# Performance work log

Hardware: AMD Instinct MI355X
Metric: run time of the kernel (lower is better)

## Reference

```python
import jax, jax.numpy as jnp
import numpy as np

NUM_USERS = 100000
NUM_ITEMS = 200000
D = 128          # embedding_dim
K = 4            # num interest heads
B = 4096
H = 256          # history length
H1, H2 = 512, 256  # hidden_units


def setup_inputs() -> dict:
    key = jax.random.key(0)
    ks = jax.random.split(key, 10)
    inp = {
        "user_ids": jax.random.randint(ks[0], (B,), 0, NUM_USERS),
        "candidate_items": jax.random.randint(ks[1], (B,), 0, NUM_ITEMS),
        "history_items": jax.random.randint(ks[2], (B, H), 0, NUM_ITEMS),
        "item_table": jax.random.normal(ks[3], (NUM_ITEMS, D), dtype=jnp.float32) * 0.05,
        "Wp": jax.random.normal(ks[4], (D, K), dtype=jnp.float32) * (1.0 / np.sqrt(D)),
        "W1": jax.random.normal(ks[5], (2 * D, H1), dtype=jnp.float32) * (1.0 / np.sqrt(2 * D)),
        "b1": jnp.zeros((H1,), dtype=jnp.float32),
        "W2": jax.random.normal(ks[6], (H1, H2), dtype=jnp.float32) * (1.0 / np.sqrt(H1)),
        "b2": jnp.zeros((H2,), dtype=jnp.float32),
        "W3": jax.random.normal(ks[7], (H2, 1), dtype=jnp.float32) * (1.0 / np.sqrt(H2)),
        "b3": jnp.zeros((1,), dtype=jnp.float32),
    }
    return inp


def reference(user_ids, candidate_items, history_items, item_table, Wp,
              W1, b1, W2, b2, W3, b3):
    # user_ids is unused by the original forward (user_emb never applied)
    item_vecs = item_table[history_items]          # (B, H, D)
    cand_vec = item_table[candidate_items]         # (B, D)

    # per-interest attention scores, softmax over history axis
    scores = jnp.einsum('bhd,dk->bhk', item_vecs, Wp)   # (B, H, K)
    scores = jax.nn.softmax(scores, axis=1)

    # softmax-weighted pooling -> K interest vectors per user
    interest_vectors = jnp.einsum('bhk,bhd->bkd', scores, item_vecs)  # (B, K, D)

    # similarity to candidate, pick best interest (data-dependent gather)
    sim_scores = jnp.einsum('bkd,bd->bk', interest_vectors, cand_vec)  # (B, K)
    best_idx = jnp.argmax(sim_scores, axis=-1)                          # (B,)
    selected = jnp.take_along_axis(
        interest_vectors, best_idx[:, None, None], axis=1)[:, 0, :]    # (B, D)

    # MLP tail: [2D -> 512] ReLU [512 -> 256] ReLU [256 -> 1], sigmoid
    x = jnp.concatenate([selected, cand_vec], axis=-1)  # (B, 2D)
    x = jax.nn.relu(x @ W1 + b1)
    x = jax.nn.relu(x @ W2 + b2)
    out = (x @ W3 + b3)[:, 0]                            # (B,)
    return jax.nn.sigmoid(out)
```

## Files before the change

### kernel.cpp

```cpp
#include <hip/hip_runtime.h>
#include <hip/hip_bf16.h>
#include <math.h>

#define B_SZ   4096
#define H_LEN  256
#define D_DIM  128
#define K_HEADS 4
#define H1_DIM 512
#define H2_DIM 256

#define CH     64
#define NCH    4
#define TPAD   132

typedef __attribute__((ext_vector_type(8))) short bf16x8;
typedef __attribute__((ext_vector_type(4))) float f32x4;

__global__ __launch_bounds__(256, 4) void interest_kernel(
    const int*   __restrict__ cand_ids,
    const int*   __restrict__ hist,
    const float* __restrict__ table,
    const float* __restrict__ Wp,
    __hip_bfloat16* __restrict__ Xbf)
{
    __shared__ float tile[CH * TPAD];
    __shared__ float wpt[K_HEADS * D_DIM];
    __shared__ float exps4[CH * 4];
    __shared__ float candv[D_DIM];
    __shared__ int   rowids[H_LEN];
    __shared__ float lsumW[16];
    __shared__ float simred[4][K_HEADS];
    __shared__ int   bestk;

    const int b    = blockIdx.x;
    const int t    = threadIdx.x;
    const int lane = t & 63, w = t >> 6;
    const int r    = t >> 2, q = t & 3;
    const int d    = t & 127, half = t >> 7;

    if (t < D_DIM) {
        float4 w4 = ((const float4*)Wp)[t];
        wpt[0 * D_DIM + t] = w4.x;
        wpt[1 * D_DIM + t] = w4.y;
        wpt[2 * D_DIM + t] = w4.z;
        wpt[3 * D_DIM + t] = w4.w;
    }
    const int cand = cand_ids[b];
    if (t >= 128 && t < 160) {
        int c = t - 128;
        ((float4*)candv)[c] = ((const float4*)(table + (long long)cand * D_DIM))[c];
    }
    rowids[t] = hist[(long long)b * H_LEN + t];

    float a0 = 0.f, a1 = 0.f, a2 = 0.f, a3 = 0.f;
    float l0 = 0.f, l1 = 0.f, l2 = 0.f, l3 = 0.f;

    for (int c = 0; c < NCH; ++c) {
        __syncthreads();

        const int   row = rowids[(c << 6) + r];
        const float* rp = table + (long long)row * D_DIM + (q << 2);
        float4 v0 = *(const float4*)(rp + 0 * 16);
        float4 v1 = *(const float4*)(rp + 1 * 16);
        float4 v2 = *(const float4*)(rp + 2 * 16);
        float4 v3 = *(const float4*)(rp + 3 * 16);
        float4 v4 = *(const float4*)(rp + 4 * 16);
        float4 v5 = *(const float4*)(rp + 5 * 16);
        float4 v6 = *(const float4*)(rp + 6 * 16);
        float4 v7 = *(const float4*)(rp + 7 * 16);

        float s0 = 0.f, s1 = 0.f, s2 = 0.f, s3 = 0.f;
        float4 va;
        #define DO_J(J, VV)                                                     \
        {   va = VV;                                                            \
            const int cb = (q << 2) + (J << 4);                                 \
            float4 w0 = *(const float4*)(wpt + 0 * D_DIM + cb);                 \
            float4 w1 = *(const float4*)(wpt + 1 * D_DIM + cb);                 \
            float4 w2 = *(const float4*)(wpt + 2 * D_DIM + cb);                 \
            float4 w3 = *(const float4*)(wpt + 3 * D_DIM + cb);                 \
            s0 += va.x * w0.x + va.y * w0.y + va.z * w0.z + va.w * w0.w;        \
            s1 += va.x * w1.x + va.y * w1.y + va.z * w1.z + va.w * w1.w;        \
            s2 += va.x * w2.x + va.y * w2.y + va.z * w2.z + va.w * w2.w;        \
            s3 += va.x * w3.x + va.y * w3.y + va.z * w3.z + va.w * w3.w;        \
            *(float4*)(tile + r * TPAD + cb) = va;                              \
        }
        DO_J(0, v0) DO_J(1, v1) DO_J(2, v2) DO_J(3, v3)
        DO_J(4, v4) DO_J(5, v5) DO_J(6, v6) DO_J(7, v7)
        #undef DO_J

        s0 += __shfl_xor(s0, 1); s0 += __shfl_xor(s0, 2);
        s1 += __shfl_xor(s1, 1); s1 += __shfl_xor(s1, 2);
        s2 += __shfl_xor(s2, 1); s2 += __shfl_xor(s2, 2);
        s3 += __shfl_xor(s3, 1); s3 += __shfl_xor(s3, 2);

        float e0 = expf(s0), e1 = expf(s1), e2 = expf(s2), e3 = expf(s3);
        if (q == 0) ((float4*)exps4)[r] = make_float4(e0, e1, e2, e3);

        float t0 = e0, t1 = e1, t2 = e2, t3 = e3;
        #pragma unroll
        for (int off = 4; off <= 32; off <<= 1) {
            t0 += __shfl_xor(t0, off);
            t1 += __shfl_xor(t1, off);
            t2 += __shfl_xor(t2, off);
            t3 += __shfl_xor(t3, off);
        }
        l0 += t0; l1 += t1; l2 += t2; l3 += t3;

        __syncthreads();

        #pragma unroll 8
        for (int i = 0; i < 32; ++i) {
            int hl = (half << 5) + i;
            float4 e4 = ((const float4*)exps4)[hl];
            float  vv = tile[hl * TPAD + d];
            a0 += e4.x * vv; a1 += e4.y * vv; a2 += e4.z * vv; a3 += e4.w * vv;
        }
    }

    __syncthreads();
    float* partBp = tile;
    float* ivbufp = tile + 512;

    if (half == 1) ((float4*)partBp)[d] = make_float4(a0, a1, a2, a3);
    if (lane == 0) ((float4*)lsumW)[w]  = make_float4(l0, l1, l2, l3);
    __syncthreads();

    float s0 = 0.f, s1 = 0.f, s2 = 0.f, s3 = 0.f;
    if (half == 0) {
        float4 pb = ((const float4*)partBp)[d];
        float4 L0 = ((const float4*)lsumW)[0];
        float4 L1 = ((const float4*)lsumW)[1];
        float4 L2 = ((const float4*)lsumW)[2];
        float4 L3 = ((const float4*)lsumW)[3];
        float i0 = 1.f / (L0.x + L1.x + L2.x + L3.x);
        float i1 = 1.f / (L0.y + L1.y + L2.y + L3.y);
        float i2 = 1.f / (L0.z + L1.z + L2.z + L3.z);
        float i3 = 1.f / (L0.w + L1.w + L2.w + L3.w);
        a0 = (a0 + pb.x) * i0;
        a1 = (a1 + pb.y) * i1;
        a2 = (a2 + pb.z) * i2;
        a3 = (a3 + pb.w) * i3;
        ((float4*)ivbufp)[d] = make_float4(a0, a1, a2, a3);
        float cd = candv[d];
        s0 = a0 * cd; s1 = a1 * cd; s2 = a2 * cd; s3 = a3 * cd;
    }
    #pragma unroll
    for (int off = 32; off >= 1; off >>= 1) {
        s0 += __shfl_xor(s0, off);
        s1 += __shfl_xor(s1, off);
        s2 += __shfl_xor(s2, off);
        s3 += __shfl_xor(s3, off);
    }
    if (lane == 0) {
        simred[w][0] = s0; simred[w][1] = s1;
        simred[w][2] = s2; simred[w][3] = s3;
    }
    __syncthreads();

    if (t == 0) {
        float sim[4];
        #pragma unroll
        for (int k = 0; k < 4; ++k)
            sim[k] = simred[0][k] + simred[1][k] + simred[2][k] + simred[3][k];
        int best = 0;
        #pragma unroll
        for (int k = 1; k < 4; ++k) if (sim[k] > sim[best]) best = k;
        bestk = best;
    }
    __syncthreads();

    __hip_bfloat16* xrow = Xbf + (long long)b * (2 * D_DIM);
    if (t < 128) xrow[t] = __float2bfloat16(ivbufp[t * 4 + bestk]);
    else         xrow[t] = __float2bfloat16(candv[t - 128]);
}

__global__ __launch_bounds__(256) void convert_weights(
    const float* __restrict__ W1, const float* __restrict__ W2,
    __hip_bfloat16* __restrict__ W1t, __hip_bfloat16* __restrict__ W2t)
{
    int idx = blockIdx.x * 256 + threadIdx.x;
    if (idx < 2 * D_DIM * H1_DIM) {
        int n = idx >> 8, k = idx & 255;
        W1t[idx] = __float2bfloat16(W1[k * H1_DIM + n]);
    } else {
        int j = idx - 2 * D_DIM * H1_DIM;
        int n = j >> 9, k = j & 511;
        W2t[j] = __float2bfloat16(W2[k * H2_DIM + n]);
    }
}

template<int N, int K, bool OUT_BF16>
__global__ __launch_bounds__(256) void mfma_mlp(
    const __hip_bfloat16* __restrict__ A,
    const __hip_bfloat16* __restrict__ Bt,
    const float* __restrict__ bias,
    void* __restrict__ Cout)
{
    const int t    = threadIdx.x;
    const int wave = t >> 6, lane = t & 63;
    const int lm   = lane & 15, quad = lane >> 4;
    const int n0   = blockIdx.x * 16;
    const int m0   = blockIdx.y * 64 + wave * 16;

    const __hip_bfloat16* Ap = A  + (long long)(m0 + lm) * K + quad * 8;
    const __hip_bfloat16* Bp = Bt + (long long)(n0 + lm) * K + quad * 8;

    f32x4 acc = {0.f, 0.f, 0.f, 0.f};
    for (int kc = 0; kc < K; kc += 256) {
        bf16x8 af[8], bfr[8];
        #pragma unroll
        for (int it = 0; it < 8; ++it) {
            af[it]  = *(const bf16x8*)(Ap + kc + it * 32);
            bfr[it] = *(const bf16x8*)(Bp + kc + it * 32);
        }
        #pragma unroll
        for (int it = 0; it < 8; ++it)
            acc = __builtin_amdgcn_mfma_f32_16x16x32_bf16(af[it], bfr[it], acc, 0, 0, 0);
    }

    const int n  = n0 + lm;
    const float bv = bias[n];
    #pragma unroll
    for (int i = 0; i < 4; ++i) {
        int m = m0 + quad * 4 + i;
        float v = fmaxf(acc[i] + bv, 0.f);
        if (OUT_BF16)
            ((__hip_bfloat16*)Cout)[(long long)m * N + n] = __float2bfloat16(v);
        else
            ((float*)Cout)[(long long)m * N + n] = v;
    }
}

__global__ __launch_bounds__(256) void head_kernel(
    const float* __restrict__ H2buf,
    const float* __restrict__ W3,
    const float* __restrict__ b3,
    float*       __restrict__ out)
{
    const int b = blockIdx.x * 256 + threadIdx.x;
    const float4* hp = (const float4*)(H2buf + (long long)b * H2_DIM);
    const float4* wp = (const float4*)W3;
    float acc = 0.f;
    #pragma unroll 8
    for (int i = 0; i < H2_DIM / 4; ++i) {
        float4 h = hp[i], wv = wp[i];
        acc += h.x * wv.x + h.y * wv.y + h.z * wv.z + h.w * wv.w;
    }
    float z = acc + b3[0];
    out[b] = 1.f / (1.f + expf(-z));
}

extern "C" void kernel_launch(void* const* d_in, const int* in_sizes, int n_in,
                              void* d_out, int out_size, void* d_ws, size_t ws_size,
                              hipStream_t stream) {
    const int*   cand  = (const int*)  d_in[1];
    const int*   hist  = (const int*)  d_in[2];
    const float* table = (const float*)d_in[3];
    const float* Wp    = (const float*)d_in[4];
    const float* W1    = (const float*)d_in[5];
    const float* b1    = (const float*)d_in[6];
    const float* W2    = (const float*)d_in[7];
    const float* b2    = (const float*)d_in[8];
    const float* W3    = (const float*)d_in[9];
    const float* b3    = (const float*)d_in[10];
    float* out = (float*)d_out;

    char* p = (char*)d_ws;
    __hip_bfloat16* Xbf  = (__hip_bfloat16*)p;                  p += (size_t)B_SZ * 2 * D_DIM * 2;
    __hip_bfloat16* Hc1  = (__hip_bfloat16*)p;                  p += (size_t)B_SZ * H1_DIM * 2;
    float*          Hc2  = (float*)p;                           p += (size_t)B_SZ * H2_DIM * 4;
    __hip_bfloat16* W1t  = (__hip_bfloat16*)p;                  p += (size_t)H1_DIM * 2 * D_DIM * 2;
    __hip_bfloat16* W2t  = (__hip_bfloat16*)p;

    convert_weights<<<(2 * D_DIM * H1_DIM + H1_DIM * H2_DIM) / 256, 256, 0, stream>>>(
        W1, W2, W1t, W2t);
    interest_kernel<<<B_SZ, 256, 0, stream>>>(cand, hist, table, Wp, Xbf);
    mfma_mlp<H1_DIM, 2 * D_DIM, true><<<dim3(H1_DIM / 16, B_SZ / 64), 256, 0, stream>>>(
        Xbf, W1t, b1, Hc1);
    mfma_mlp<H2_DIM, H1_DIM, false><<<dim3(H2_DIM / 16, B_SZ / 64), 256, 0, stream>>>(
        Hc1, W2t, b2, Hc2);
    head_kernel<<<B_SZ / 256, 256, 0, stream>>>(Hc2, W3, b3, out);
}
```

Before: 274.8 us.

## Make interest pooling wave-local with register prefetch and fuse weight conversion

The interest kernel is restructured so that each wave owns its own 16-row tile slice and does its own weighted pooling. This removes the block-wide barriers inside the history loop, and cross-wave partials are reduced once at the end. The next chunk of gathered table rows is prefetched into registers while the current chunk is being processed, to hide gather latency. The separate weight-conversion kernel is folded into extra blocks of the interest kernel, saving one launch. The cost is higher register pressure from the double-buffered float4 arrays, which may reduce occupancy.

```diff
diff --git a/kernel.cpp b/kernel.cpp
--- a/kernel.cpp
+++ b/kernel.cpp
@@ -8,9 +8,6 @@
 #define K_HEADS 4
 #define H1_DIM 512
 #define H2_DIM 256
-
-#define CH     64
-#define NCH    4
 #define TPAD   132
 
 typedef __attribute__((ext_vector_type(8))) short bf16x8;
@@ -21,13 +18,30 @@
     const int*   __restrict__ hist,
     const float* __restrict__ table,
     const float* __restrict__ Wp,
+    const float* __restrict__ W1,
+    const float* __restrict__ W2,
+    __hip_bfloat16* __restrict__ W1t,
+    __hip_bfloat16* __restrict__ W2t,
     __hip_bfloat16* __restrict__ Xbf)
 {
-    __shared__ float tile[CH * TPAD];
+    if (blockIdx.x >= B_SZ) {
+        int idx = (blockIdx.x - B_SZ) * 256 + threadIdx.x;
+        if (idx < 2 * D_DIM * H1_DIM) {
+            int n = idx >> 8, k = idx & 255;
+            W1t[idx] = __float2bfloat16(W1[k * H1_DIM + n]);
+        } else {
+            int j = idx - 2 * D_DIM * H1_DIM;
+            int n = j >> 9, k = j & 511;
+            W2t[j] = __float2bfloat16(W2[k * H2_DIM + n]);
+        }
+        return;
+    }
+
+    __shared__ float tile[4 * 16 * TPAD];
     __shared__ float wpt[K_HEADS * D_DIM];
-    __shared__ float exps4[CH * 4];
+    __shared__ float exps4[4 * 16 * 4];
     __shared__ float candv[D_DIM];
-    __shared__ int   rowids[H_LEN];
+    __shared__ float ivbuf[D_DIM * 4];
     __shared__ float lsumW[16];
     __shared__ float simred[4][K_HEADS];
     __shared__ int   bestk;
@@ -35,8 +49,10 @@
     const int b    = blockIdx.x;
     const int t    = threadIdx.x;
     const int lane = t & 63, w = t >> 6;
-    const int r    = t >> 2, q = t & 3;
-    const int d    = t & 127, half = t >> 7;
+    const int r    = lane >> 2;
+    const int q    = lane & 3;
+    const int d0   = lane, d1 = lane + 64;
+    const int wtile = w * (16 * TPAD);
 
     if (t < D_DIM) {
         float4 w4 = ((const float4*)Wp)[t];
@@ -50,84 +66,97 @@
         int c = t - 128;
         ((float4*)candv)[c] = ((const float4*)(table + (long long)cand * D_DIM))[c];
     }
-    rowids[t] = hist[(long long)b * H_LEN + t];
-
-    float a0 = 0.f, a1 = 0.f, a2 = 0.f, a3 = 0.f;
-    float l0 = 0.f, l1 = 0.f, l2 = 0.f, l3 = 0.f;
-
-    for (int c = 0; c < NCH; ++c) {
-        __syncthreads();
-
-        const int   row = rowids[(c << 6) + r];
-        const float* rp = table + (long long)row * D_DIM + (q << 2);
-        float4 v0 = *(const float4*)(rp + 0 * 16);
-        float4 v1 = *(const float4*)(rp + 1 * 16);
-        float4 v2 = *(const float4*)(rp + 2 * 16);
-        float4 v3 = *(const float4*)(rp + 3 * 16);
-        float4 v4 = *(const float4*)(rp + 4 * 16);
-        float4 v5 = *(const float4*)(rp + 5 * 16);
-        float4 v6 = *(const float4*)(rp + 6 * 16);
-        float4 v7 = *(const float4*)(rp + 7 * 16);
-
+    __syncthreads();
+
+    int ids[4];
+    {
+        const long long hb = (long long)b * H_LEN + w * 64 + r;
+        #pragma unroll
+        for (int c = 0; c < 4; ++c) ids[c] = hist[hb + c * 16];
+    }
+
+    float accA[4] = {0.f, 0.f, 0.f, 0.f};
+    float accB[4] = {0.f, 0.f, 0.f, 0.f};
+    float lsum[4] = {0.f, 0.f, 0.f, 0.f};
+
+    float4 v[8];
+    {
+        const float* rp = table + (long long)ids[0] * D_DIM + (q << 2);
+        #pragma unroll
+        for (int j = 0; j < 8; ++j) v[j] = *(const float4*)(rp + j * 16);
+    }
+
+    #pragma unroll
+    for (int c = 0; c < 4; ++c) {
         float s0 = 0.f, s1 = 0.f, s2 = 0.f, s3 = 0.f;
-        float4 va;
-        #define DO_J(J, VV)                                                     \
-        {   va = VV;                                                            \
-            const int cb = (q << 2) + (J << 4);                                 \
-            float4 w0 = *(const float4*)(wpt + 0 * D_DIM + cb);                 \
-            float4 w1 = *(const float4*)(wpt + 1 * D_DIM + cb);                 \
-            float4 w2 = *(const float4*)(wpt + 2 * D_DIM + cb);                 \
-            float4 w3 = *(const float4*)(wpt + 3 * D_DIM + cb);                 \
-            s0 += va.x * w0.x + va.y * w0.y + va.z * w0.z + va.w * w0.w;        \
-            s1 += va.x * w1.x + va.y * w1.y + va.z * w1.z + va.w * w1.w;        \
-            s2 += va.x * w2.x + va.y * w2.y + va.z * w2.z + va.w * w2.w;        \
-            s3 += va.x * w3.x + va.y * w3.y + va.z * w3.z + va.w * w3.w;        \
-            *(float4*)(tile + r * TPAD + cb) = va;                              \
-        }
-        DO_J(0, v0) DO_J(1, v1) DO_J(2, v2) DO_J(3, v3)
-        DO_J(4, v4) DO_J(5, v5) DO_J(6, v6) DO_J(7, v7)
-        #undef DO_J
+        #pragma unroll
+        for (int j = 0; j < 8; ++j) {
+            const int cb = (q << 2) + (j << 4);
+            float4 va = v[j];
+            float4 w0 = *(const float4*)(wpt + 0 * D_DIM + cb);
+            float4 w1 = *(const float4*)(wpt + 1 * D_DIM + cb);
+            float4 w2 = *(const float4*)(wpt + 2 * D_DIM + cb);
+            float4 w3 = *(const float4*)(wpt + 3 * D_DIM + cb);
+            s0 += va.x * w0.x + va.y * w0.y + va.z * w0.z + va.w * w0.w;
+            s1 += va.x * w1.x + va.y * w1.y + va.z * w1.z + va.w * w1.w;
+            s2 += va.x * w2.x + va.y * w2.y + va.z * w2.z + va.w * w2.w;
+            s3 += va.x * w3.x + va.y * w3.y + va.z * w3.z + va.w * w3.w;
+            *(float4*)(tile + wtile + r * TPAD + cb) = va;
+        }
+
+        float4 vn[8];
+        if (c < 3) {
+            const float* rp = table + (long long)ids[c + 1] * D_DIM + (q << 2);
+            #pragma unroll
+            for (int j = 0; j < 8; ++j) vn[j] = *(const float4*)(rp + j * 16);
+        }
 
         s0 += __shfl_xor(s0, 1); s0 += __shfl_xor(s0, 2);
         s1 += __shfl_xor(s1, 1); s1 += __shfl_xor(s1, 2);
         s2 += __shfl_xor(s2, 1); s2 += __shfl_xor(s2, 2);
         s3 += __shfl_xor(s3, 1); s3 += __shfl_xor(s3, 2);
-
         float e0 = expf(s0), e1 = expf(s1), e2 = expf(s2), e3 = expf(s3);
-        if (q == 0) ((float4*)exps4)[r] = make_float4(e0, e1, e2, e3);
-
-        float t0 = e0, t1 = e1, t2 = e2, t3 = e3;
-        #pragma unroll
-        for (int off = 4; off <= 32; off <<= 1) {
-            t0 += __shfl_xor(t0, off);
-            t1 += __shfl_xor(t1, off);
-            t2 += __shfl_xor(t2, off);
-            t3 += __shfl_xor(t3, off);
-        }
-        l0 += t0; l1 += t1; l2 += t2; l3 += t3;
-
-        __syncthreads();
-
-        #pragma unroll 8
-        for (int i = 0; i < 32; ++i) {
-            int hl = (half << 5) + i;
-            float4 e4 = ((const float4*)exps4)[hl];
-            float  vv = tile[hl * TPAD + d];
-            a0 += e4.x * vv; a1 += e4.y * vv; a2 += e4.z * vv; a3 += e4.w * vv;
-        }
-    }
-
-    __syncthreads();
-    float* partBp = tile;
-    float* ivbufp = tile + 512;
-
-    if (half == 1) ((float4*)partBp)[d] = make_float4(a0, a1, a2, a3);
-    if (lane == 0) ((float4*)lsumW)[w]  = make_float4(l0, l1, l2, l3);
+        if (q == 0) ((float4*)exps4)[w * 16 + r] = make_float4(e0, e1, e2, e3);
+        lsum[0] += e0; lsum[1] += e1; lsum[2] += e2; lsum[3] += e3;
+
+        #pragma unroll
+        for (int h = 0; h < 16; ++h) {
+            float4 e4 = ((const float4*)exps4)[w * 16 + h];
+            float  p0 = tile[wtile + h * TPAD + d0];
+            float  p1 = tile[wtile + h * TPAD + d1];
+            accA[0] += e4.x * p0; accA[1] += e4.y * p0;
+            accA[2] += e4.z * p0; accA[3] += e4.w * p0;
+            accB[0] += e4.x * p1; accB[1] += e4.y * p1;
+            accB[2] += e4.z * p1; accB[3] += e4.w * p1;
+        }
+
+        if (c < 3) {
+            #pragma unroll
+            for (int j = 0; j < 8; ++j) v[j] = vn[j];
+        }
+    }
+
+    #pragma unroll
+    for (int off = 4; off <= 32; off <<= 1) {
+        lsum[0] += __shfl_xor(lsum[0], off);
+        lsum[1] += __shfl_xor(lsum[1], off);
+        lsum[2] += __shfl_xor(lsum[2], off);
+        lsum[3] += __shfl_xor(lsum[3], off);
+    }
+
+    float* Pw = tile + wtile;
+    ((float4*)Pw)[d0] = make_float4(accA[0], accA[1], accA[2], accA[3]);
+    ((float4*)Pw)[d1] = make_float4(accB[0], accB[1], accB[2], accB[3]);
+    if (lane == 0) ((float4*)lsumW)[w] = make_float4(lsum[0], lsum[1], lsum[2], lsum[3]);
     __syncthreads();
 
     float s0 = 0.f, s1 = 0.f, s2 = 0.f, s3 = 0.f;
-    if (half == 0) {
-        float4 pb = ((const float4*)partBp)[d];
+    if (t < 128) {
+        const int d = t;
+        float4 p0 = ((const float4*)(tile + 0 * 16 * TPAD))[d];
+        float4 p1 = ((const float4*)(tile + 1 * 16 * TPAD))[d];
+        float4 p2 = ((const float4*)(tile + 2 * 16 * TPAD))[d];
+        float4 p3 = ((const float4*)(tile + 3 * 16 * TPAD))[d];
         float4 L0 = ((const float4*)lsumW)[0];
         float4 L1 = ((const float4*)lsumW)[1];
         float4 L2 = ((const float4*)lsumW)[2];
@@ -136,11 +165,11 @@
         float i1 = 1.f / (L0.y + L1.y + L2.y + L3.y);
         float i2 = 1.f / (L0.z + L1.z + L2.z + L3.z);
         float i3 = 1.f / (L0.w + L1.w + L2.w + L3.w);
-        a0 = (a0 + pb.x) * i0;
-        a1 = (a1 + pb.y) * i1;
-        a2 = (a2 + pb.z) * i2;
-        a3 = (a3 + pb.w) * i3;
-        ((float4*)ivbufp)[d] = make_float4(a0, a1, a2, a3);
+        float a0 = (((p0.x + p1.x) + p2.x) + p3.x) * i0;
+        float a1 = (((p0.y + p1.y) + p2.y) + p3.y) * i1;
+        float a2 = (((p0.z + p1.z) + p2.z) + p3.z) * i2;
+        float a3 = (((p0.w + p1.w) + p2.w) + p3.w) * i3;
+        ((float4*)ivbuf)[d] = make_float4(a0, a1, a2, a3);
         float cd = candv[d];
         s0 = a0 * cd; s1 = a1 * cd; s2 = a2 * cd; s3 = a3 * cd;
     }
@@ -170,23 +199,8 @@
     __syncthreads();
 
     __hip_bfloat16* xrow = Xbf + (long long)b * (2 * D_DIM);
-    if (t < 128) xrow[t] = __float2bfloat16(ivbufp[t * 4 + bestk]);
+    if (t < 128) xrow[t] = __float2bfloat16(ivbuf[t * 4 + bestk]);
     else         xrow[t] = __float2bfloat16(candv[t - 128]);
-}
-
-__global__ __launch_bounds__(256) void convert_weights(
-    const float* __restrict__ W1, const float* __restrict__ W2,
-    __hip_bfloat16* __restrict__ W1t, __hip_bfloat16* __restrict__ W2t)
-{
-    int idx = blockIdx.x * 256 + threadIdx.x;
-    if (idx < 2 * D_DIM * H1_DIM) {
-        int n = idx >> 8, k = idx & 255;
-        W1t[idx] = __float2bfloat16(W1[k * H1_DIM + n]);
-    } else {
-        int j = idx - 2 * D_DIM * H1_DIM;
-        int n = j >> 9, k = j & 511;
-        W2t[j] = __float2bfloat16(W2[k * H2_DIM + n]);
-    }
 }
 
 template<int N, int K, bool OUT_BF16>
@@ -272,9 +286,8 @@
     __hip_bfloat16* W1t  = (__hip_bfloat16*)p;                  p += (size_t)H1_DIM * 2 * D_DIM * 2;
     __hip_bfloat16* W2t  = (__hip_bfloat16*)p;
 
-    convert_weights<<<(2 * D_DIM * H1_DIM + H1_DIM * H2_DIM) / 256, 256, 0, stream>>>(
-        W1, W2, W1t, W2t);
-    interest_kernel<<<B_SZ, 256, 0, stream>>>(cand, hist, table, Wp, Xbf);
+    interest_kernel<<<B_SZ + 1024, 256, 0, stream>>>(
+        cand, hist, table, Wp, W1, W2, W1t, W2t, Xbf);
     mfma_mlp<H1_DIM, 2 * D_DIM, true><<<dim3(H1_DIM / 16, B_SZ / 64), 256, 0, stream>>>(
         Xbf, W1t, b1, Hc1);
     mfma_mlp<H2_DIM, H1_DIM, false><<<dim3(H2_DIM / 16, B_SZ / 64), 256, 0, stream>>>(
```

Result: slower. 730.2 us (+165.8%).

## Fuse MLP layers and head into one kernel, fold weight conversion into interest kernel

Applied to the files above, without the earlier changes.

Merges the two MFMA GEMM layers, bias/ReLU and the final W3 dot plus sigmoid into a single kernel that keeps the 64x512 hidden tile in LDS. This removes the global round-trips for the H1 and H2 activations and cuts two launches. Weight transpose/convert is also folded into extra blocks of the interest kernel, which removes one more launch. The cost is that the fused MLP runs only 64 blocks, each looping over all N tiles and reloading full W1t/W2t from cache, so parallelism on the MLP tail drops sharply.

```diff
diff --git a/kernel.cpp b/kernel.cpp
--- a/kernel.cpp
+++ b/kernel.cpp
@@ -12,6 +12,7 @@
 #define CH     64
 #define NCH    4
 #define TPAD   132
+#define H1PAD  520
 
 typedef __attribute__((ext_vector_type(8))) short bf16x8;
 typedef __attribute__((ext_vector_type(4))) float f32x4;
@@ -21,8 +22,25 @@
     const int*   __restrict__ hist,
     const float* __restrict__ table,
     const float* __restrict__ Wp,
+    const float* __restrict__ W1,
+    const float* __restrict__ W2,
+    __hip_bfloat16* __restrict__ W1t,
+    __hip_bfloat16* __restrict__ W2t,
     __hip_bfloat16* __restrict__ Xbf)
 {
+    if (blockIdx.x >= B_SZ) {
+        int idx = (blockIdx.x - B_SZ) * 256 + threadIdx.x;
+        if (idx < 2 * D_DIM * H1_DIM) {
+            int n = idx >> 8, k = idx & 255;
+            W1t[idx] = __float2bfloat16(W1[k * H1_DIM + n]);
+        } else {
+            int j = idx - 2 * D_DIM * H1_DIM;
+            int n = j >> 9, k = j & 511;
+            W2t[j] = __float2bfloat16(W2[k * H2_DIM + n]);
+        }
+        return;
+    }
+
     __shared__ float tile[CH * TPAD];
     __shared__ float wpt[K_HEADS * D_DIM];
     __shared__ float exps4[CH * 4];
@@ -174,80 +192,84 @@
     else         xrow[t] = __float2bfloat16(candv[t - 128]);
 }
 
-__global__ __launch_bounds__(256) void convert_weights(
-    const float* __restrict__ W1, const float* __restrict__ W2,
-    __hip_bfloat16* __restrict__ W1t, __hip_bfloat16* __restrict__ W2t)
+__global__ __launch_bounds__(256) void fused_mlp(
+    const __hip_bfloat16* __restrict__ Xbf,
+    const __hip_bfloat16* __restrict__ W1t,
+    const float* __restrict__ b1,
+    const __hip_bfloat16* __restrict__ W2t,
+    const float* __restrict__ b2,
+    const float* __restrict__ W3,
+    const float* __restrict__ b3,
+    float* __restrict__ out)
 {
-    int idx = blockIdx.x * 256 + threadIdx.x;
-    if (idx < 2 * D_DIM * H1_DIM) {
-        int n = idx >> 8, k = idx & 255;
-        W1t[idx] = __float2bfloat16(W1[k * H1_DIM + n]);
-    } else {
-        int j = idx - 2 * D_DIM * H1_DIM;
-        int n = j >> 9, k = j & 511;
-        W2t[j] = __float2bfloat16(W2[k * H2_DIM + n]);
-    }
-}
-
-template<int N, int K, bool OUT_BF16>
-__global__ __launch_bounds__(256) void mfma_mlp(
-    const __hip_bfloat16* __restrict__ A,
-    const __hip_bfloat16* __restrict__ Bt,
-    const float* __restrict__ bias,
-    void* __restrict__ Cout)
-{
+    __shared__ __hip_bfloat16 H1s[64 * H1PAD];
+
     const int t    = threadIdx.x;
     const int wave = t >> 6, lane = t & 63;
     const int lm   = lane & 15, quad = lane >> 4;
-    const int n0   = blockIdx.x * 16;
-    const int m0   = blockIdx.y * 64 + wave * 16;
-
-    const __hip_bfloat16* Ap = A  + (long long)(m0 + lm) * K + quad * 8;
-    const __hip_bfloat16* Bp = Bt + (long long)(n0 + lm) * K + quad * 8;
-
-    f32x4 acc = {0.f, 0.f, 0.f, 0.f};
-    for (int kc = 0; kc < K; kc += 256) {
-        bf16x8 af[8], bfr[8];
-        #pragma unroll
-        for (int it = 0; it < 8; ++it) {
-            af[it]  = *(const bf16x8*)(Ap + kc + it * 32);
-            bfr[it] = *(const bf16x8*)(Bp + kc + it * 32);
-        }
-        #pragma unroll
-        for (int it = 0; it < 8; ++it)
-            acc = __builtin_amdgcn_mfma_f32_16x16x32_bf16(af[it], bfr[it], acc, 0, 0, 0);
-    }
-
-    const int n  = n0 + lm;
-    const float bv = bias[n];
-    #pragma unroll
-    for (int i = 0; i < 4; ++i) {
-        int m = m0 + quad * 4 + i;
-        float v = fmaxf(acc[i] + bv, 0.f);
-        if (OUT_BF16)
-            ((__hip_bfloat16*)Cout)[(long long)m * N + n] = __float2bfloat16(v);
-        else
-            ((float*)Cout)[(long long)m * N + n] = v;
-    }
-}
-
-__global__ __launch_bounds__(256) void head_kernel(
-    const float* __restrict__ H2buf,
-    const float* __restrict__ W3,
-    const float* __restrict__ b3,
-    float*       __restrict__ out)
-{
-    const int b = blockIdx.x * 256 + threadIdx.x;
-    const float4* hp = (const float4*)(H2buf + (long long)b * H2_DIM);
-    const float4* wp = (const float4*)W3;
-    float acc = 0.f;
-    #pragma unroll 8
-    for (int i = 0; i < H2_DIM / 4; ++i) {
-        float4 h = hp[i], wv = wp[i];
-        acc += h.x * wv.x + h.y * wv.y + h.z * wv.z + h.w * wv.w;
-    }
-    float z = acc + b3[0];
-    out[b] = 1.f / (1.f + expf(-z));
+    const int mrow = blockIdx.x * 64 + wave * 16;
+    const int lrow = wave * 16;
+
+    const __hip_bfloat16* Ap = Xbf + (long long)(mrow + lm) * 256 + quad * 8;
+    bf16x8 afr[8];
+    #pragma unroll
+    for (int j = 0; j < 8; ++j) afr[j] = *(const bf16x8*)(Ap + j * 32);
+
+    #pragma unroll 4
+    for (int nt = 0; nt < 32; ++nt) {
+        const int n = nt * 16 + lm;
+        const __hip_bfloat16* Bp = W1t + (long long)n * 256 + quad * 8;
+        f32x4 acc = {0.f, 0.f, 0.f, 0.f};
+        #pragma unroll
+        for (int j = 0; j < 8; ++j) {
+            bf16x8 bfr = *(const bf16x8*)(Bp + j * 32);
+            acc = __builtin_amdgcn_mfma_f32_16x16x32_bf16(afr[j], bfr, acc, 0, 0, 0);
+        }
+        const float bv = b1[n];
+        #pragma unroll
+        for (int i = 0; i < 4; ++i) {
+            float v = fmaxf(acc[i] + bv, 0.f);
+            H1s[(lrow + quad * 4 + i) * H1PAD + n] = __float2bfloat16(v);
+        }
+    }
+
+    bf16x8 hfr[16];
+    #pragma unroll
+    for (int j = 0; j < 16; ++j)
+        hfr[j] = *(const bf16x8*)(&H1s[(lrow + lm) * H1PAD + j * 32 + quad * 8]);
+
+    float hp[4] = {0.f, 0.f, 0.f, 0.f};
+    #pragma unroll 2
+    for (int nt = 0; nt < 16; ++nt) {
+        const int n = nt * 16 + lm;
+        const __hip_bfloat16* Bp = W2t + (long long)n * 512 + quad * 8;
+        f32x4 acc = {0.f, 0.f, 0.f, 0.f};
+        #pragma unroll
+        for (int j = 0; j < 16; ++j) {
+            bf16x8 bfr = *(const bf16x8*)(Bp + j * 32);
+            acc = __builtin_amdgcn_mfma_f32_16x16x32_bf16(hfr[j], bfr, acc, 0, 0, 0);
+        }
+        const float bv = b2[n], w3v = W3[n];
+        #pragma unroll
+        for (int i = 0; i < 4; ++i)
+            hp[i] += fmaxf(acc[i] + bv, 0.f) * w3v;
+    }
+
+    #pragma unroll
+    for (int off = 1; off <= 8; off <<= 1) {
+        hp[0] += __shfl_xor(hp[0], off);
+        hp[1] += __shfl_xor(hp[1], off);
+        hp[2] += __shfl_xor(hp[2], off);
+        hp[3] += __shfl_xor(hp[3], off);
+    }
+    if (lm == 0) {
+        const float bb = b3[0];
+        #pragma unroll
+        for (int i = 0; i < 4; ++i) {
+            float z = hp[i] + bb;
+            out[mrow + quad * 4 + i] = 1.f / (1.f + expf(-z));
+        }
+    }
 }
 
 extern "C" void kernel_launch(void* const* d_in, const int* in_sizes, int n_in,
@@ -266,18 +288,11 @@
     float* out = (float*)d_out;
 
     char* p = (char*)d_ws;
-    __hip_bfloat16* Xbf  = (__hip_bfloat16*)p;                  p += (size_t)B_SZ * 2 * D_DIM * 2;
-    __hip_bfloat16* Hc1  = (__hip_bfloat16*)p;                  p += (size_t)B_SZ * H1_DIM * 2;
-    float*          Hc2  = (float*)p;                           p += (size_t)B_SZ * H2_DIM * 4;
-    __hip_bfloat16* W1t  = (__hip_bfloat16*)p;                  p += (size_t)H1_DIM * 2 * D_DIM * 2;
-    __hip_bfloat16* W2t  = (__hip_bfloat16*)p;
-
-    convert_weights<<<(2 * D_DIM * H1_DIM + H1_DIM * H2_DIM) / 256, 256, 0, stream>>>(
-        W1, W2, W1t, W2t);
-    interest_kernel<<<B_SZ, 256, 0, stream>>>(cand, hist, table, Wp, Xbf);
-    mfma_mlp<H1_DIM, 2 * D_DIM, true><<<dim3(H1_DIM / 16, B_SZ / 64), 256, 0, stream>>>(
-        Xbf, W1t, b1, Hc1);
-    mfma_mlp<H2_DIM, H1_DIM, false><<<dim3(H2_DIM / 16, B_SZ / 64), 256, 0, stream>>>(
-        Hc1, W2t, b2, Hc2);
-    head_kernel<<<B_SZ / 256, 256, 0, stream>>>(Hc2, W3, b3, out);
+    __hip_bfloat16* Xbf = (__hip_bfloat16*)p;  p += (size_t)B_SZ * 2 * D_DIM * 2;
+    __hip_bfloat16* W1t = (__hip_bfloat16*)p;  p += (size_t)H1_DIM * 2 * D_DIM * 2;
+    __hip_bfloat16* W2t = (__hip_bfloat16*)p;
+
+    interest_kernel<<<B_SZ + 1024, 256, 0, stream>>>(
+        cand, hist, table, Wp, W1, W2, W1t, W2t, Xbf);
+    fused_mlp<<<B_SZ / 64, 256, 0, stream>>>(Xbf, W1t, b1, W2t, b2, W3, b3, out);
 }
```

Result: slower. 297.1 us (+8.1%).
